# Performance work log

Hardware: AMD Instinct MI355X
Metric: run time of the kernel (lower is better)

The kernel has to match this reference:

```python
import jax, jax.numpy as jnp
import numpy as np
import itertools, math

B = 2048
DIM = 384
RES = 7
KEY_DIM = 16
HEADS = 8
RATIO = 4
NH_KD = KEY_DIM * HEADS          # 128
D = RATIO * KEY_DIM              # 64
DH = D * HEADS                   # 512
OUT_DIM = DIM                    # 384
RES2 = math.ceil(RES / 2)        # 4
N = RES * RES                    # 49
N2 = RES2 * RES2                 # 16
EPS = 1e-5
SCALE = KEY_DIM ** -0.5


def conv2d(x, w, b, stride=1, pad=0, groups=1):
    out = jax.lax.conv_general_dilated(
        x, w, (stride, stride), [(pad, pad), (pad, pad)],
        dimension_numbers=("NCHW", "OIHW", "NCHW"), feature_group_count=groups)
    return out + b[None, :, None, None]


def bn(x, p):
    # p: [4, C] = (gamma, beta, running_mean, running_var); inference-mode BN
    g, be, m, v = p[0], p[1], p[2], p[3]
    inv = jax.lax.rsqrt(v + EPS)
    return (x - m[None, :, None, None]) * (g * inv)[None, :, None, None] + be[None, :, None, None]


def avgpool2(x):
    # AvgPool2d(kernel=2, stride=2, padding=0)
    s = jax.lax.reduce_window(x, 0.0, jax.lax.add, (1, 1, 2, 2), (1, 1, 2, 2), "VALID")
    return s * 0.25


def _bias_idxs():
    points = list(itertools.product(range(RES), range(RES)))
    points_ = list(itertools.product(range(RES2), range(RES2)))
    stride = RES / RES2
    offsets, idxs = {}, []
    for p1 in points_:
        for p2 in points:
            off = (math.floor(abs(p1[0] * stride - p2[0])),
                   math.floor(abs(p1[1] * stride - p2[1])))
            if off not in offsets:
                offsets[off] = len(offsets)
            idxs.append(offsets[off])
    return np.array(idxs, dtype=np.int32).reshape(N2, N), len(offsets)


def _bn_params(k, c):
    k1, k2, k3, k4 = jax.random.split(k, 4)
    gamma = 1.0 + 0.1 * jax.random.normal(k1, (c,), jnp.float32)
    beta = 0.1 * jax.random.normal(k2, (c,), jnp.float32)
    mean = 0.1 * jax.random.normal(k3, (c,), jnp.float32)
    var = jax.random.uniform(k4, (c,), jnp.float32, 0.5, 1.5)
    return jnp.stack([gamma, beta, mean, var])


def _conv_w(k, shape):
    fan_in = shape[1] * shape[2] * shape[3]
    return jax.random.normal(k, shape, jnp.float32) / np.sqrt(fan_in)


def setup_inputs() -> dict:
    key = jax.random.key(0)
    ks = jax.random.split(key, 20)
    idxs_np, n_off = _bias_idxs()
    inp = {
        "x": jax.random.normal(ks[0], (B, DIM, RES, RES), jnp.float32),
        # LGQuery: depthwise 3x3 s2 + proj 1x1 + BN
        "qlw": _conv_w(ks[1], (DIM, 1, 3, 3)),
        "qlb": 0.01 * jax.random.normal(ks[2], (DIM,), jnp.float32),
        "qpw": _conv_w(ks[3], (NH_KD, DIM, 1, 1)),
        "qpb": 0.01 * jax.random.normal(ks[4], (NH_KD,), jnp.float32),
        "qbn": _bn_params(ks[5], NH_KD),
        # K branch: 1x1 conv + BN
        "kw": _conv_w(ks[6], (NH_KD, DIM, 1, 1)),
        "kb": 0.01 * jax.random.normal(ks[7], (NH_KD,), jnp.float32),
        "kbn": _bn_params(ks[8], NH_KD),
        # V branch: 1x1 conv + BN
        "vw": _conv_w(ks[9], (DH, DIM, 1, 1)),
        "vb": 0.01 * jax.random.normal(ks[10], (DH,), jnp.float32),
        "vbn": _bn_params(ks[11], DH),
        # v_local: depthwise 3x3 s2 + BN
        "vlw": _conv_w(ks[12], (DH, 1, 3, 3)),
        "vlb": 0.01 * jax.random.normal(ks[13], (DH,), jnp.float32),
        "vlbn": _bn_params(ks[14], DH),
        # proj: ReLU -> 1x1 conv -> BN
        "pw": _conv_w(ks[15], (OUT_DIM, DH, 1, 1)),
        "pb": 0.01 * jax.random.normal(ks[16], (OUT_DIM,), jnp.float32),
        "pbn": _bn_params(ks[17], OUT_DIM),
        # relative position biases + gather indices
        "ab": 0.02 * jax.random.normal(ks[18], (HEADS, n_off), jnp.float32),
        "bias_idxs": jnp.asarray(idxs_np),
    }
    return inp


def reference(x, qlw, qlb, qpw, qpb, qbn, kw, kb, kbn, vw, vb, vbn,
              vlw, vlb, vlbn, pw, pb, pbn, ab, bias_idxs):
    Bx = x.shape[0]
    # --- LGQuery ---
    local_q = conv2d(x, qlw, qlb, stride=2, pad=1, groups=DIM)   # [B,384,4,4]
    pool_q = avgpool2(x)                                         # [B,384,3,3]
    ph = local_q.shape[-2] - pool_q.shape[-2]
    pw_ = local_q.shape[-1] - pool_q.shape[-1]
    if ph > 0 or pw_ > 0:
        pool_q = jnp.pad(pool_q, ((0, 0), (0, 0), (0, ph), (0, pw_)))
    q_out = bn(conv2d(local_q + pool_q, qpw, qpb), qbn)          # [B,128,4,4]
    Hq, Wq = q_out.shape[-2], q_out.shape[-1]
    Nq = Hq * Wq
    # --- K / V ---
    k_out = bn(conv2d(x, kw, kb), kbn)                           # [B,128,7,7]
    Nk = k_out.shape[-2] * k_out.shape[-1]
    v_out = bn(conv2d(x, vw, vb), vbn)                           # [B,512,7,7]
    v_loc = bn(conv2d(v_out, vlw, vlb, stride=2, pad=1, groups=DH), vlbn)  # [B,512,4,4]
    # --- attention over tiny 16x49 matrices per head ---
    q = q_out.reshape(Bx, HEADS, KEY_DIM, Nq)                    # [B,H,kd,Nq]
    k = k_out.reshape(Bx, HEADS, KEY_DIM, Nk)                    # [B,H,kd,Nk]
    v = v_out.reshape(Bx, HEADS, D, Nk)                          # [B,H,d,Nk]
    attn = jnp.einsum("bhdq,bhdk->bhqk", q, k) * SCALE           # [B,H,16,49]
    if Nq == N2 and Nk == N:
        attn = attn + ab[:, bias_idxs]                           # gather -> [H,16,49]
    attn = jax.nn.softmax(attn, axis=-1)
    xa = jnp.einsum("bhqk,bhdk->bhdq", attn, v)                  # [B,H,d,Nq]
    out = xa.reshape(Bx, DH, Hq, Wq)                             # [B,512,4,4]
    ph2 = out.shape[-2] - v_loc.shape[-2]
    pw2 = out.shape[-1] - v_loc.shape[-1]
    if ph2 > 0 or pw2 > 0:
        v_loc = jnp.pad(v_loc, ((0, 0), (0, 0), (0, ph2), (0, pw2)))
    out = out + v_loc
    out = bn(conv2d(jax.nn.relu(out), pw, pb), pbn)              # [B,384,4,4]
    return out
```

## Files before the change

### kernel.cpp

```cpp
#include <hip/hip_runtime.h>
#include <hip/hip_bf16.h>


#define DIMC 384
#define NPOS 49
#define NHKD 128
#define DHC  512
#define OUTC 384

#define OFF_KW  0
#define OFF_VW  49152
#define OFF_QPW 245760
#define OFF_PW  294912
#define W_TOT   491520

#define XS_OFF 0
#define R0_OFF 19208
#define R1_OFF 27528
#define R2_OFF 32648
#define SMEM_ELEMS 40840

typedef __attribute__((ext_vector_type(8))) __bf16 bf16x8;
typedef __attribute__((ext_vector_type(4))) float f32x4;

static __device__ __forceinline__ __hip_bfloat16 f2b(float x) { return __float2bfloat16(x); }
static __device__ __forceinline__ float b2f(__hip_bfloat16 x) { return __bfloat162float(x); }
static __device__ __forceinline__ bf16x8 ld8(const __hip_bfloat16* p) { return *(const bf16x8*)p; }
static __device__ __forceinline__ f32x4 fzero() {
  f32x4 z; z[0] = 0.f; z[1] = 0.f; z[2] = 0.f; z[3] = 0.f; return z;
}
static __device__ __forceinline__ bf16x8 bzero() {
  bf16x8 z;
  #pragma unroll
  for (int j = 0; j < 8; ++j) z[j] = (__bf16)0.0f;
  return z;
}

static __device__ __forceinline__ void bn_so(const float* bn, int C, int ch,
                                             float convb, float& s, float& o) {
  float g  = bn[ch];
  float be = bn[C + ch];
  float mu = bn[2*C + ch];
  float va = bn[3*C + ch];
  s = g * rsqrtf(va + 1e-5f);
  o = be + (convb - mu) * s;
}

__global__ void prep_weights(const float* __restrict__ kw, const float* __restrict__ vw,
                             const float* __restrict__ qpw, const float* __restrict__ pw,
                             __hip_bfloat16* __restrict__ wsb) {
  for (int i = blockIdx.x * blockDim.x + threadIdx.x; i < W_TOT; i += gridDim.x * blockDim.x) {
    float v;
    if (i < OFF_VW)       v = kw[i - OFF_KW];
    else if (i < OFF_QPW) v = vw[i - OFF_VW];
    else if (i < OFF_PW)  v = qpw[i - OFF_QPW];
    else                  v = pw[i - OFF_PW];
    wsb[i] = f2b(v);
  }
}

__global__ __launch_bounds__(512, 4) void attn4d_kernel(
    const float* __restrict__ x,
    const float* __restrict__ qlw, const float* __restrict__ qlb,
    const float* __restrict__ qpb, const float* __restrict__ qbn,
    const float* __restrict__ kb,  const float* __restrict__ kbn,
    const float* __restrict__ vb,  const float* __restrict__ vbn,
    const float* __restrict__ vlw, const float* __restrict__ vlb,
    const float* __restrict__ vlbn,
    const float* __restrict__ pb,  const float* __restrict__ pbn,
    const float* __restrict__ ab,  const int* __restrict__ bidx,
    const __hip_bfloat16* __restrict__ wsb,
    int n_off, float* __restrict__ out)
{
  __shared__ __align__(16) __hip_bfloat16 smem[SMEM_ELEMS];
  __hip_bfloat16* xs    = smem + XS_OFF;
  __hip_bfloat16* vsm   = smem + XS_OFF;
  __hip_bfloat16* kt    = smem + R0_OFF;
  __hip_bfloat16* rout  = smem + R0_OFF;
  __hip_bfloat16* qsm   = smem + R1_OFF;
  __hip_bfloat16* qin   = smem + R2_OFF;
  __hip_bfloat16* attnS = smem + R2_OFF;

  const __hip_bfloat16* kwb  = wsb + OFF_KW;
  const __hip_bfloat16* vwb  = wsb + OFF_VW;
  const __hip_bfloat16* qpwb = wsb + OFF_QPW;
  const __hip_bfloat16* pwb  = wsb + OFF_PW;

  const int tid  = threadIdx.x;
  const int lane = tid & 63;
  const int wave = tid >> 6;
  const int quad = lane >> 4;
  const int l15  = lane & 15;
  const int b    = blockIdx.x;

  {
    const float* xg = x + (size_t)b * (DIMC * NPOS);
    for (int j = tid; j < NPOS * (DIMC / 8); j += 512) {
      const int n  = j % 49;
      const int c0 = (j / 49) * 8;
      union { bf16x8 v; __hip_bfloat16 h[8]; } u;
      #pragma unroll
      for (int k = 0; k < 8; ++k)
        u.h[k] = f2b(xg[(c0 + k) * 49 + n]);
      *(bf16x8*)&xs[n * 392 + c0] = u.v;
    }
  }
  __syncthreads();

  if (tid < DIMC) {
    const int c = tid;
    float xv[49];
    #pragma unroll
    for (int n = 0; n < 49; ++n) xv[n] = b2f(xs[n * 392 + c]);
    float wq[9];
    #pragma unroll
    for (int j = 0; j < 9; ++j) wq[j] = qlw[c * 9 + j];
    const float cb = qlb[c];
    #pragma unroll
    for (int oh = 0; oh < 4; ++oh) {
      #pragma unroll
      for (int ow = 0; ow < 4; ++ow) {
        float a = cb;
        #pragma unroll
        for (int kh = 0; kh < 3; ++kh) {
          const int ih = 2 * oh - 1 + kh;
          if (ih < 0 || ih > 6) continue;
          #pragma unroll
          for (int kwi = 0; kwi < 3; ++kwi) {
            const int iw = 2 * ow - 1 + kwi;
            if (iw < 0 || iw > 6) continue;
            a += wq[kh * 3 + kwi] * xv[ih * 7 + iw];
          }
        }
        if (oh < 3 && ow < 3)
          a += 0.25f * (xv[(2*oh)*7 + 2*ow] + xv[(2*oh)*7 + 2*ow + 1] +
                        xv[(2*oh+1)*7 + 2*ow] + xv[(2*oh+1)*7 + 2*ow + 1]);
        qin[(oh * 4 + ow) * 392 + c] = f2b(a);
      }
    }
  }
  __syncthreads();


  {
    const int mt = wave;
    f32x4 acc[4];
    #pragma unroll
    for (int nt = 0; nt < 4; ++nt) acc[nt] = fzero();
    for (int ks = 0; ks < 12; ++ks) {
      const int c0 = ks * 32 + quad * 8;
      bf16x8 a = ld8(&kwb[(mt * 16 + l15) * DIMC + c0]);
      bf16x8 z[4];
      #pragma unroll
      for (int nt = 0; nt < 3; ++nt) z[nt] = ld8(&xs[(nt * 16 + l15) * 392 + c0]);
      z[3] = (l15 == 0) ? ld8(&xs[48 * 392 + c0]) : bzero();
      #pragma unroll
      for (int nt = 0; nt < 4; ++nt)
        acc[nt] = __builtin_amdgcn_mfma_f32_16x16x32_bf16(a, z[nt], acc[nt], 0, 0, 0);
    }
    #pragma unroll
    for (int r = 0; r < 4; ++r) {
      const int oc = mt * 16 + quad * 4 + r;
      float s, o;
      bn_so(kbn, NHKD, oc, kb[oc], s, o);
      #pragma unroll
      for (int nt = 0; nt < 4; ++nt) {
        const int n = nt * 16 + l15;
        if (n < 49) kt[n * 136 + oc] = f2b(acc[nt][r] * s + o);
      }
    }
  }

  {
    const int mt = wave;
    f32x4 acc = fzero();
    for (int ks = 0; ks < 12; ++ks) {
      const int c0 = ks * 32 + quad * 8;
      bf16x8 bv = ld8(&qin[l15 * 392 + c0]);
      bf16x8 av = ld8(&qpwb[(mt * 16 + l15) * DIMC + c0]);
      acc = __builtin_amdgcn_mfma_f32_16x16x32_bf16(av, bv, acc, 0, 0, 0);
    }
    #pragma unroll
    for (int r = 0; r < 4; ++r) {
      const int oc = mt * 16 + quad * 4 + r;
      float s, o;
      bn_so(qbn, NHKD, oc, qpb[oc], s, o);
      const int kd = oc & 15;
      qsm[wave * 640 + l15 * 40 + kd] = f2b(acc[r] * s + o);
      qsm[wave * 640 + l15 * 40 + kd + 16] = f2b(0.f);
    }
  }

  f32x4 va[2][2][4];
  #pragma unroll
  for (int p = 0; p < 2; ++p)
    #pragma unroll
    for (int mt = 0; mt < 2; ++mt)
      #pragma unroll
      for (int nt = 0; nt < 4; ++nt) va[p][mt][nt] = fzero();
  {
    const int chb = wave * 32;
    for (int ks = 0; ks < 12; ++ks) {
      const int c0 = ks * 32 + quad * 8;
      bf16x8 z[4];
      #pragma unroll
      for (int nt = 0; nt < 3; ++nt) z[nt] = ld8(&xs[(nt * 16 + l15) * 392 + c0]);
      z[3] = (l15 == 0) ? ld8(&xs[48 * 392 + c0]) : bzero();
      #pragma unroll
      for (int p = 0; p < 2; ++p) {
        #pragma unroll
        for (int mt = 0; mt < 2; ++mt) {
          bf16x8 a = ld8(&vwb[(p * 256 + chb + mt * 16 + l15) * DIMC + c0]);
          #pragma unroll
          for (int nt = 0; nt < 4; ++nt)
            va[p][mt][nt] = __builtin_amdgcn_mfma_f32_16x16x32_bf16(a, z[nt], va[p][mt][nt], 0, 0, 0);
        }
      }
    }
  }
  __syncthreads();

  {
    __hip_bfloat16* vbw_ = vsm + wave * 2304;
    #pragma unroll
    for (int mt = 0; mt < 2; ++mt)
      #pragma unroll
      for (int r = 0; r < 4; ++r) {
        const int chl = mt * 16 + quad * 4 + r;
        const int gch = wave * 32 + chl;
        float s, o;
        bn_so(vbn, DHC, gch, vb[gch], s, o);
        #pragma unroll
        for (int nt = 0; nt < 4; ++nt)
          vbw_[chl * 72 + nt * 16 + l15] = f2b(va[0][mt][nt][r] * s + o);
      }
  }

  {
    const int h = wave;
    bf16x8 av = ld8(&qsm[h * 640 + l15 * 40 + quad * 8]);
    float p[4][4];
    #pragma unroll
    for (int t = 0; t < 4; ++t) {
      bf16x8 bv = bzero();
      if (quad < 2) bv = ld8(&kt[(t * 16 + l15) * 136 + h * 16 + quad * 8]);
      f32x4 lg = __builtin_amdgcn_mfma_f32_16x16x32_bf16(av, bv, fzero(), 0, 0, 0);
      #pragma unroll
      for (int r = 0; r < 4; ++r) {
        const int nq = quad * 4 + r;
        const int nk = t * 16 + l15;
        float val = -30000.f;
        if (nk < 49) val = lg[r] * 0.25f + ab[h * n_off + bidx[nq * 49 + nk]];
        p[t][r] = val;
      }
    }
    #pragma unroll
    for (int r = 0; r < 4; ++r) {
      float m = fmaxf(fmaxf(p[0][r], p[1][r]), fmaxf(p[2][r], p[3][r]));
      m = fmaxf(m, __shfl_xor(m, 1));
      m = fmaxf(m, __shfl_xor(m, 2));
      m = fmaxf(m, __shfl_xor(m, 4));
      m = fmaxf(m, __shfl_xor(m, 8));
      float e[4], sum = 0.f;
      #pragma unroll
      for (int t = 0; t < 4; ++t) { e[t] = __expf(p[t][r] - m); sum += e[t]; }
      sum += __shfl_xor(sum, 1);
      sum += __shfl_xor(sum, 2);
      sum += __shfl_xor(sum, 4);
      sum += __shfl_xor(sum, 8);
      const float inv = 1.f / sum;
      #pragma unroll
      for (int t = 0; t < 4; ++t) p[t][r] = e[t] * inv;
    }
    #pragma unroll
    for (int r = 0; r < 4; ++r) {
      const int nq = quad * 4 + r;
      #pragma unroll
      for (int t = 0; t < 4; ++t) {
        const int nk = t * 16 + l15;
        attnS[h * 1024 + nq * 64 + (nk ^ ((nq & 7) << 3))] = f2b(p[t][r]);
      }
    }
  }
  __syncthreads();

  #pragma unroll
  for (int p = 0; p < 2; ++p) {
    if (p == 1) {
      __hip_bfloat16* vbw_ = vsm + wave * 2304;
      #pragma unroll
      for (int mt = 0; mt < 2; ++mt)
        #pragma unroll
        for (int r = 0; r < 4; ++r) {
          const int chl = mt * 16 + quad * 4 + r;
          const int gch = 256 + wave * 32 + chl;
          float s, o;
          bn_so(vbn, DHC, gch, vb[gch], s, o);
          #pragma unroll
          for (int nt = 0; nt < 4; ++nt)
            vbw_[chl * 72 + nt * 16 + l15] = f2b(va[1][mt][nt][r] * s + o);
        }
    }

    {
      const int cl   = lane & 31;
      const int half = lane >> 5;
      const int gch  = p * 256 + wave * 32 + cl;
      const __hip_bfloat16* vrow = vsm + wave * 2304 + cl * 72;
      float wv[9];
      #pragma unroll
      for (int j = 0; j < 9; ++j) wv[j] = vlw[gch * 9 + j];
      float s, o;
      bn_so(vlbn, DHC, gch, vlb[gch], s, o);
      #pragma unroll
      for (int pp = 0; pp < 8; ++pp) {
        const int pos = half * 8 + pp;
        const int oh = pos >> 2, ow = pos & 3;
        float a = 0.f;
        #pragma unroll
        for (int kh = 0; kh < 3; ++kh) {
          const int ih = 2 * oh - 1 + kh;
          if (ih < 0 || ih > 6) continue;
          #pragma unroll
          for (int kwi = 0; kwi < 3; ++kwi) {
            const int iw = 2 * ow - 1 + kwi;
            if (iw < 0 || iw > 6) continue;
            a += wv[kh * 3 + kwi] * b2f(vrow[ih * 7 + iw]);
          }
        }
        rout[pos * 520 + gch] = f2b(a * s + o);
      }
    }

    {
      const int h = p * 4 + (wave >> 1);
      const __hip_bfloat16* vbw_ = vsm + wave * 2304;
      #pragma unroll
      for (int mt = 0; mt < 2; ++mt) {
        f32x4 acc = fzero();
        #pragma unroll
        for (int ks = 0; ks < 2; ++ks) {
          const int k0 = ks * 32 + quad * 8;
          bf16x8 av = ld8(&vbw_[(mt * 16 + l15) * 72 + k0]);
          bf16x8 bv = ld8(&attnS[h * 1024 + l15 * 64 + (k0 ^ ((l15 & 7) << 3))]);
          acc = __builtin_amdgcn_mfma_f32_16x16x32_bf16(av, bv, acc, 0, 0, 0);
        }
        #pragma unroll
        for (int r = 0; r < 4; ++r) {
          const int gch = p * 256 + wave * 32 + mt * 16 + quad * 4 + r;
          const int ad = l15 * 520 + gch;
          const float val = acc[r] + b2f(rout[ad]);
          rout[ad] = f2b(fmaxf(val, 0.f));
        }
      }
    }
  }
  __syncthreads();

  {
    const int mt0 = wave * 3;
    f32x4 acc[3];
    #pragma unroll
    for (int t = 0; t < 3; ++t) acc[t] = fzero();
    for (int ks = 0; ks < 16; ++ks) {
      const int c0 = ks * 32 + quad * 8;
      bf16x8 bv = ld8(&rout[l15 * 520 + c0]);
      #pragma unroll
      for (int t = 0; t < 3; ++t) {
        bf16x8 av = ld8(&pwb[((mt0 + t) * 16 + l15) * DHC + c0]);
        acc[t] = __builtin_amdgcn_mfma_f32_16x16x32_bf16(av, bv, acc[t], 0, 0, 0);
      }
    }
    float* outb = out + (size_t)b * (OUTC * 16);
    #pragma unroll
    for (int t = 0; t < 3; ++t) {
      #pragma unroll
      for (int r = 0; r < 4; ++r) {
        const int oc = (mt0 + t) * 16 + quad * 4 + r;
        float s, o;
        bn_so(pbn, OUTC, oc, pb[oc], s, o);
        outb[oc * 16 + l15] = acc[t][r] * s + o;
      }
    }
  }
}

extern "C" void kernel_launch(void* const* d_in, const int* in_sizes, int n_in,
                              void* d_out, int out_size, void* d_ws, size_t ws_size,
                              hipStream_t stream) {
  const float* x    = (const float*)d_in[0];
  const float* qlw  = (const float*)d_in[1];
  const float* qlb  = (const float*)d_in[2];
  const float* qpw  = (const float*)d_in[3];
  const float* qpb  = (const float*)d_in[4];
  const float* qbn  = (const float*)d_in[5];
  const float* kw   = (const float*)d_in[6];
  const float* kb   = (const float*)d_in[7];
  const float* kbn  = (const float*)d_in[8];
  const float* vw   = (const float*)d_in[9];
  const float* vb   = (const float*)d_in[10];
  const float* vbn  = (const float*)d_in[11];
  const float* vlw  = (const float*)d_in[12];
  const float* vlb  = (const float*)d_in[13];
  const float* vlbn = (const float*)d_in[14];
  const float* pw   = (const float*)d_in[15];
  const float* pb   = (const float*)d_in[16];
  const float* pbn  = (const float*)d_in[17];
  const float* ab   = (const float*)d_in[18];
  const int*   bidx = (const int*)d_in[19];
  const int n_off = in_sizes[18] / 8;
  const int Bn = in_sizes[0] / (DIMC * NPOS);

  __hip_bfloat16* wsb = (__hip_bfloat16*)d_ws;

  prep_weights<<<480, 256, 0, stream>>>(kw, vw, qpw, pw, wsb);
  attn4d_kernel<<<Bn, 512, 0, stream>>>(x, qlw, qlb, qpb, qbn, kb, kbn,
                                        vb, vbn, vlw, vlb, vlbn, pb, pbn,
                                        ab, bidx, wsb, n_off, (float*)d_out);
}
```

Measured before the change: 580.2 us.

## Precompute BN scale/offset and gathered attention bias in prep kernel; shrink LDS

Folds every batch-norm scale/shift and conv bias into a float2 table, and gathers the attention bias into a dense per-head table, both computed once in the weight-prep kernel rather than in every block. The main kernel reads these precomputed values, removing per-block rsqrt work and indirect gathers. It also shrinks the padded q buffer to lower LDS use, restructures the q depthwise conv to keep only three rows in registers, and preloads v rows as vector loads for the v-local conv. The cost is a slightly larger prep kernel and a different LDS layout.

```diff
diff --git a/kernel.cpp b/kernel.cpp
--- a/kernel.cpp
+++ b/kernel.cpp
@@ -13,12 +13,19 @@
 #define OFF_QPW 245760
 #define OFF_PW  294912
 #define W_TOT   491520
-
-#define XS_OFF 0
-#define R0_OFF 19208
-#define R1_OFF 27528
-#define R2_OFF 32648
-#define SMEM_ELEMS 40840
+#define BN_K  0
+#define BN_Q  128
+#define BN_V  256
+#define BN_VL 768
+#define BN_P  1280
+#define BN_TOT 1664
+#define ABF_ELEMS (8 * 784)
+
+#define XS_OFF   0
+#define KT_OFF   19208
+#define QSM_OFF  27912
+#define QIN_OFF  29960
+#define SMEM_ELEMS 38152
 
 typedef __attribute__((ext_vector_type(8))) __bf16 bf16x8;
 typedef __attribute__((ext_vector_type(4))) float f32x4;
@@ -36,20 +43,19 @@
   return z;
 }
 
-static __device__ __forceinline__ void bn_so(const float* bn, int C, int ch,
-                                             float convb, float& s, float& o) {
-  float g  = bn[ch];
-  float be = bn[C + ch];
-  float mu = bn[2*C + ch];
-  float va = bn[3*C + ch];
-  s = g * rsqrtf(va + 1e-5f);
-  o = be + (convb - mu) * s;
-}
-
 __global__ void prep_weights(const float* __restrict__ kw, const float* __restrict__ vw,
                              const float* __restrict__ qpw, const float* __restrict__ pw,
+                             const float* __restrict__ kb,  const float* __restrict__ kbn,
+                             const float* __restrict__ qpb, const float* __restrict__ qbn,
+                             const float* __restrict__ vb,  const float* __restrict__ vbn,
+                             const float* __restrict__ vlb, const float* __restrict__ vlbn,
+                             const float* __restrict__ pb,  const float* __restrict__ pbn,
+                             const float* __restrict__ ab,  const int* __restrict__ bidx,
+                             int n_off,
                              __hip_bfloat16* __restrict__ wsb) {
-  for (int i = blockIdx.x * blockDim.x + threadIdx.x; i < W_TOT; i += gridDim.x * blockDim.x) {
+  const int gid = blockIdx.x * blockDim.x + threadIdx.x;
+  const int stride = gridDim.x * blockDim.x;
+  for (int i = gid; i < W_TOT; i += stride) {
     float v;
     if (i < OFF_VW)       v = kw[i - OFF_KW];
     else if (i < OFF_QPW) v = vw[i - OFF_VW];
@@ -57,34 +63,47 @@
     else                  v = pw[i - OFF_PW];
     wsb[i] = f2b(v);
   }
+  float2* bnt = (float2*)(wsb + W_TOT);
+  for (int i = gid; i < BN_TOT; i += stride) {
+    const float *bn, *cb; int ch, C;
+    if (i < BN_Q)        { bn = kbn;  cb = kb;  ch = i;         C = NHKD; }
+    else if (i < BN_V)   { bn = qbn;  cb = qpb; ch = i - BN_Q;  C = NHKD; }
+    else if (i < BN_VL)  { bn = vbn;  cb = vb;  ch = i - BN_V;  C = DHC;  }
+    else if (i < BN_P)   { bn = vlbn; cb = vlb; ch = i - BN_VL; C = DHC;  }
+    else                 { bn = pbn;  cb = pb;  ch = i - BN_P;  C = OUTC; }
+    const float g = bn[ch], be = bn[C + ch], mu = bn[2*C + ch], va = bn[3*C + ch];
+    const float s = g * rsqrtf(va + 1e-5f);
+    bnt[i] = make_float2(s, be + (cb[ch] - mu) * s);
+  }
+  float* abf = (float*)((char*)bnt + BN_TOT * 8);
+  for (int i = gid; i < ABF_ELEMS; i += stride) {
+    const int h = i / 784, j = i - h * 784;
+    abf[i] = ab[h * n_off + bidx[j]];
+  }
 }
 
 __global__ __launch_bounds__(512, 4) void attn4d_kernel(
     const float* __restrict__ x,
     const float* __restrict__ qlw, const float* __restrict__ qlb,
-    const float* __restrict__ qpb, const float* __restrict__ qbn,
-    const float* __restrict__ kb,  const float* __restrict__ kbn,
-    const float* __restrict__ vb,  const float* __restrict__ vbn,
-    const float* __restrict__ vlw, const float* __restrict__ vlb,
-    const float* __restrict__ vlbn,
-    const float* __restrict__ pb,  const float* __restrict__ pbn,
-    const float* __restrict__ ab,  const int* __restrict__ bidx,
+    const float* __restrict__ vlw,
     const __hip_bfloat16* __restrict__ wsb,
-    int n_off, float* __restrict__ out)
+    float* __restrict__ out)
 {
   __shared__ __align__(16) __hip_bfloat16 smem[SMEM_ELEMS];
   __hip_bfloat16* xs    = smem + XS_OFF;
   __hip_bfloat16* vsm   = smem + XS_OFF;
-  __hip_bfloat16* kt    = smem + R0_OFF;
-  __hip_bfloat16* rout  = smem + R0_OFF;
-  __hip_bfloat16* qsm   = smem + R1_OFF;
-  __hip_bfloat16* qin   = smem + R2_OFF;
-  __hip_bfloat16* attnS = smem + R2_OFF;
+  __hip_bfloat16* kt    = smem + KT_OFF;
+  __hip_bfloat16* rout  = smem + KT_OFF;
+  __hip_bfloat16* qsm   = smem + QSM_OFF;
+  __hip_bfloat16* qin   = smem + QIN_OFF;
+  __hip_bfloat16* attnS = smem + QIN_OFF;
 
   const __hip_bfloat16* kwb  = wsb + OFF_KW;
   const __hip_bfloat16* vwb  = wsb + OFF_VW;
   const __hip_bfloat16* qpwb = wsb + OFF_QPW;
   const __hip_bfloat16* pwb  = wsb + OFF_PW;
+  const float2* bnt = (const float2*)(wsb + W_TOT);
+  const float*  abf = (const float*)((const char*)bnt + BN_TOT * 8);
 
   const int tid  = threadIdx.x;
   const int lane = tid & 63;
@@ -98,29 +117,219 @@
     for (int j = tid; j < NPOS * (DIMC / 8); j += 512) {
       const int n  = j % 49;
       const int c0 = (j / 49) * 8;
-      union { bf16x8 v; __hip_bfloat16 h[8]; } u;
+      bf16x8 v;
       #pragma unroll
       for (int k = 0; k < 8; ++k)
-        u.h[k] = f2b(xg[(c0 + k) * 49 + n]);
-      *(bf16x8*)&xs[n * 392 + c0] = u.v;
+        v[k] = (__bf16)(xg[(c0 + k) * 49 + n]);
+      *(bf16x8*)&xs[n * 392 + c0] = v;
     }
   }
   __syncthreads();
 
-  if (tid < DIMC) {
+  if (tid < 384) {
     const int c = tid;
-    float xv[49];
-    #pragma unroll
-    for (int n = 0; n < 49; ++n) xv[n] = b2f(xs[n * 392 + c]);
     float wq[9];
     #pragma unroll
     for (int j = 0; j < 9; ++j) wq[j] = qlw[c * 9 + j];
     const float cb = qlb[c];
     #pragma unroll
     for (int oh = 0; oh < 4; ++oh) {
+      float w[3][7];
+      #pragma unroll
+      for (int i = 0; i < 7; ++i) {
+        w[0][i] = (oh > 0) ? b2f(xs[((2*oh - 1) * 7 + i) * 392 + c]) : 0.f;
+        w[1][i] = b2f(xs[((2*oh) * 7 + i) * 392 + c]);
+        w[2][i] = (oh < 3) ? b2f(xs[((2*oh + 1) * 7 + i) * 392 + c]) : 0.f;
+      }
       #pragma unroll
       for (int ow = 0; ow < 4; ++ow) {
         float a = cb;
+        #pragma unroll
+        for (int kh = 0; kh < 3; ++kh) {
+          #pragma unroll
+          for (int kwi = 0; kwi < 3; ++kwi) {
+            const int iw = 2 * ow - 1 + kwi;
+            if (iw < 0 || iw > 6) continue;
+            a += wq[kh * 3 + kwi] * w[kh][iw];
+          }
+        }
+        if (oh < 3 && ow < 3)
+          a += 0.25f * (w[1][2*ow] + w[1][2*ow + 1] + w[2][2*ow] + w[2][2*ow + 1]);
+        qin[(oh * 4 + ow) * 392 + c] = f2b(a);
+      }
+    }
+  }
+  __syncthreads();
+
+
+  {
+    const int mt = wave;
+    f32x4 acc[4];
+    #pragma unroll
+    for (int nt = 0; nt < 4; ++nt) acc[nt] = fzero();
+    for (int ks = 0; ks < 12; ++ks) {
+      const int c0 = ks * 32 + quad * 8;
+      bf16x8 a = ld8(&kwb[(mt * 16 + l15) * DIMC + c0]);
+      bf16x8 z[4];
+      #pragma unroll
+      for (int nt = 0; nt < 3; ++nt) z[nt] = ld8(&xs[(nt * 16 + l15) * 392 + c0]);
+      z[3] = (l15 == 0) ? ld8(&xs[48 * 392 + c0]) : bzero();
+      #pragma unroll
+      for (int nt = 0; nt < 4; ++nt)
+        acc[nt] = __builtin_amdgcn_mfma_f32_16x16x32_bf16(a, z[nt], acc[nt], 0, 0, 0);
+    }
+    #pragma unroll
+    for (int r = 0; r < 4; ++r) {
+      const int oc = mt * 16 + quad * 4 + r;
+      const float2 so = bnt[BN_K + oc];
+      #pragma unroll
+      for (int nt = 0; nt < 4; ++nt) {
+        const int n = nt * 16 + l15;
+        if (n < 49) kt[n * 136 + oc] = f2b(acc[nt][r] * so.x + so.y);
+      }
+    }
+  }
+
+  {
+    const int mt = wave;
+    f32x4 acc = fzero();
+    for (int ks = 0; ks < 12; ++ks) {
+      const int c0 = ks * 32 + quad * 8;
+      bf16x8 bv = ld8(&qin[l15 * 392 + c0]);
+      bf16x8 av = ld8(&qpwb[(mt * 16 + l15) * DIMC + c0]);
+      acc = __builtin_amdgcn_mfma_f32_16x16x32_bf16(av, bv, acc, 0, 0, 0);
+    }
+    #pragma unroll
+    for (int r = 0; r < 4; ++r) {
+      const int oc = mt * 16 + quad * 4 + r;
+      const float2 so = bnt[BN_Q + oc];
+      qsm[mt * 256 + l15 * 16 + (oc & 15)] = f2b(acc[r] * so.x + so.y);
+    }
+  }
+
+  f32x4 va[2][2][4];
+  #pragma unroll
+  for (int p = 0; p < 2; ++p)
+    #pragma unroll
+    for (int mt = 0; mt < 2; ++mt)
+      #pragma unroll
+      for (int nt = 0; nt < 4; ++nt) va[p][mt][nt] = fzero();
+  {
+    const int chb = wave * 32;
+    for (int ks = 0; ks < 12; ++ks) {
+      const int c0 = ks * 32 + quad * 8;
+      bf16x8 z[4];
+      #pragma unroll
+      for (int nt = 0; nt < 3; ++nt) z[nt] = ld8(&xs[(nt * 16 + l15) * 392 + c0]);
+      z[3] = (l15 == 0) ? ld8(&xs[48 * 392 + c0]) : bzero();
+      #pragma unroll
+      for (int p = 0; p < 2; ++p) {
+        #pragma unroll
+        for (int mt = 0; mt < 2; ++mt) {
+          bf16x8 a = ld8(&vwb[(p * 256 + chb + mt * 16 + l15) * DIMC + c0]);
+          #pragma unroll
+          for (int nt = 0; nt < 4; ++nt)
+            va[p][mt][nt] = __builtin_amdgcn_mfma_f32_16x16x32_bf16(a, z[nt], va[p][mt][nt], 0, 0, 0);
+        }
+      }
+    }
+  }
+  __syncthreads();
+
+  {
+    __hip_bfloat16* vbw_ = vsm + wave * 2304;
+    #pragma unroll
+    for (int mt = 0; mt < 2; ++mt)
+      #pragma unroll
+      for (int r = 0; r < 4; ++r) {
+        const int chl = mt * 16 + quad * 4 + r;
+        const float2 so = bnt[BN_V + wave * 32 + chl];
+        #pragma unroll
+        for (int nt = 0; nt < 4; ++nt)
+          vbw_[chl * 72 + nt * 16 + l15] = f2b(va[0][mt][nt][r] * so.x + so.y);
+      }
+  }
+
+  {
+    const int h = wave;
+    bf16x8 av = (quad < 2) ? ld8(&qsm[h * 256 + l15 * 16 + quad * 8]) : bzero();
+    float p[4][4];
+    #pragma unroll
+    for (int t = 0; t < 4; ++t) {
+      bf16x8 bv = (quad < 2) ? ld8(&kt[(t * 16 + l15) * 136 + h * 16 + quad * 8]) : bzero();
+      f32x4 lg = __builtin_amdgcn_mfma_f32_16x16x32_bf16(av, bv, fzero(), 0, 0, 0);
+      #pragma unroll
+      for (int r = 0; r < 4; ++r) {
+        const int nq = quad * 4 + r;
+        const int nk = t * 16 + l15;
+        float val = -30000.f;
+        if (nk < 49) val = lg[r] * 0.25f + abf[h * 784 + nq * 49 + nk];
+        p[t][r] = val;
+      }
+    }
+    #pragma unroll
+    for (int r = 0; r < 4; ++r) {
+      float m = fmaxf(fmaxf(p[0][r], p[1][r]), fmaxf(p[2][r], p[3][r]));
+      m = fmaxf(m, __shfl_xor(m, 1));
+      m = fmaxf(m, __shfl_xor(m, 2));
+      m = fmaxf(m, __shfl_xor(m, 4));
+      m = fmaxf(m, __shfl_xor(m, 8));
+      float e[4], sum = 0.f;
+      #pragma unroll
+      for (int t = 0; t < 4; ++t) { e[t] = __expf(p[t][r] - m); sum += e[t]; }
+      sum += __shfl_xor(sum, 1);
+      sum += __shfl_xor(sum, 2);
+      sum += __shfl_xor(sum, 4);
+      sum += __shfl_xor(sum, 8);
+      const float inv = 1.f / sum;
+      #pragma unroll
+      for (int t = 0; t < 4; ++t) p[t][r] = e[t] * inv;
+    }
+    #pragma unroll
+    for (int r = 0; r < 4; ++r) {
+      const int nq = quad * 4 + r;
+      #pragma unroll
+      for (int t = 0; t < 4; ++t) {
+        const int nk = t * 16 + l15;
+        attnS[h * 1024 + nq * 64 + (nk ^ ((nq & 7) << 3))] = f2b(p[t][r]);
+      }
+    }
+  }
+  __syncthreads();
+
+  #pragma unroll
+  for (int p = 0; p < 2; ++p) {
+    if (p == 1) {
+      __hip_bfloat16* vbw_ = vsm + wave * 2304;
+      #pragma unroll
+      for (int mt = 0; mt < 2; ++mt)
+        #pragma unroll
+        for (int r = 0; r < 4; ++r) {
+          const int chl = mt * 16 + quad * 4 + r;
+          const float2 so = bnt[BN_V + 256 + wave * 32 + chl];
+          #pragma unroll
+          for (int nt = 0; nt < 4; ++nt)
+            vbw_[chl * 72 + nt * 16 + l15] = f2b(va[1][mt][nt][r] * so.x + so.y);
+        }
+    }
+
+    {
+      const int cl   = lane & 31;
+      const int half = lane >> 5;
+      const int gch  = p * 256 + wave * 32 + cl;
+      const __hip_bfloat16* vrow = vsm + wave * 2304 + cl * 72;
+      bf16x8 rv[7];
+      #pragma unroll
+      for (int t = 0; t < 7; ++t) rv[t] = ld8(vrow + t * 8);
+      float wv[9];
+      #pragma unroll
+      for (int j = 0; j < 9; ++j) wv[j] = vlw[gch * 9 + j];
+      const float2 so = bnt[BN_VL + gch];
+      #pragma unroll
+      for (int pp = 0; pp < 8; ++pp) {
+        const int pos = half * 8 + pp;
+        const int oh = pos >> 2, ow = pos & 3;
+        float a = 0.f;
         #pragma unroll
         for (int kh = 0; kh < 3; ++kh) {
           const int ih = 2 * oh - 1 + kh;
@@ -129,206 +338,11 @@
           for (int kwi = 0; kwi < 3; ++kwi) {
             const int iw = 2 * ow - 1 + kwi;
             if (iw < 0 || iw > 6) continue;
-            a += wq[kh * 3 + kwi] * xv[ih * 7 + iw];
+            const int e = ih * 7 + iw;
+            a += wv[kh * 3 + kwi] * (float)rv[e >> 3][e & 7];
           }
         }
-        if (oh < 3 && ow < 3)
-          a += 0.25f * (xv[(2*oh)*7 + 2*ow] + xv[(2*oh)*7 + 2*ow + 1] +
-                        xv[(2*oh+1)*7 + 2*ow] + xv[(2*oh+1)*7 + 2*ow + 1]);
-        qin[(oh * 4 + ow) * 392 + c] = f2b(a);
-      }
-    }
-  }
-  __syncthreads();
-
-
-  {
-    const int mt = wave;
-    f32x4 acc[4];
-    #pragma unroll
-    for (int nt = 0; nt < 4; ++nt) acc[nt] = fzero();
-    for (int ks = 0; ks < 12; ++ks) {
-      const int c0 = ks * 32 + quad * 8;
-      bf16x8 a = ld8(&kwb[(mt * 16 + l15) * DIMC + c0]);
-      bf16x8 z[4];
-      #pragma unroll
-      for (int nt = 0; nt < 3; ++nt) z[nt] = ld8(&xs[(nt * 16 + l15) * 392 + c0]);
-      z[3] = (l15 == 0) ? ld8(&xs[48 * 392 + c0]) : bzero();
-      #pragma unroll
-      for (int nt = 0; nt < 4; ++nt)
-        acc[nt] = __builtin_amdgcn_mfma_f32_16x16x32_bf16(a, z[nt], acc[nt], 0, 0, 0);
-    }
-    #pragma unroll
-    for (int r = 0; r < 4; ++r) {
-      const int oc = mt * 16 + quad * 4 + r;
-      float s, o;
-      bn_so(kbn, NHKD, oc, kb[oc], s, o);
-      #pragma unroll
-      for (int nt = 0; nt < 4; ++nt) {
-        const int n = nt * 16 + l15;
-        if (n < 49) kt[n * 136 + oc] = f2b(acc[nt][r] * s + o);
-      }
-    }
-  }
-
-  {
-    const int mt = wave;
-    f32x4 acc = fzero();
-    for (int ks = 0; ks < 12; ++ks) {
-      const int c0 = ks * 32 + quad * 8;
-      bf16x8 bv = ld8(&qin[l15 * 392 + c0]);
-      bf16x8 av = ld8(&qpwb[(mt * 16 + l15) * DIMC + c0]);
-      acc = __builtin_amdgcn_mfma_f32_16x16x32_bf16(av, bv, acc, 0, 0, 0);
-    }
-    #pragma unroll
-    for (int r = 0; r < 4; ++r) {
-      const int oc = mt * 16 + quad * 4 + r;
-      float s, o;
-      bn_so(qbn, NHKD, oc, qpb[oc], s, o);
-      const int kd = oc & 15;
-      qsm[wave * 640 + l15 * 40 + kd] = f2b(acc[r] * s + o);
-      qsm[wave * 640 + l15 * 40 + kd + 16] = f2b(0.f);
-    }
-  }
-
-  f32x4 va[2][2][4];
-  #pragma unroll
-  for (int p = 0; p < 2; ++p)
-    #pragma unroll
-    for (int mt = 0; mt < 2; ++mt)
-      #pragma unroll
-      for (int nt = 0; nt < 4; ++nt) va[p][mt][nt] = fzero();
-  {
-    const int chb = wave * 32;
-    for (int ks = 0; ks < 12; ++ks) {
-      const int c0 = ks * 32 + quad * 8;
-      bf16x8 z[4];
-      #pragma unroll
-      for (int nt = 0; nt < 3; ++nt) z[nt] = ld8(&xs[(nt * 16 + l15) * 392 + c0]);
-      z[3] = (l15 == 0) ? ld8(&xs[48 * 392 + c0]) : bzero();
-      #pragma unroll
-      for (int p = 0; p < 2; ++p) {
-        #pragma unroll
-        for (int mt = 0; mt < 2; ++mt) {
-          bf16x8 a = ld8(&vwb[(p * 256 + chb + mt * 16 + l15) * DIMC + c0]);
-          #pragma unroll
-          for (int nt = 0; nt < 4; ++nt)
-            va[p][mt][nt] = __builtin_amdgcn_mfma_f32_16x16x32_bf16(a, z[nt], va[p][mt][nt], 0, 0, 0);
-        }
-      }
-    }
-  }
-  __syncthreads();
-
-  {
-    __hip_bfloat16* vbw_ = vsm + wave * 2304;
-    #pragma unroll
-    for (int mt = 0; mt < 2; ++mt)
-      #pragma unroll
-      for (int r = 0; r < 4; ++r) {
-        const int chl = mt * 16 + quad * 4 + r;
-        const int gch = wave * 32 + chl;
-        float s, o;
-        bn_so(vbn, DHC, gch, vb[gch], s, o);
-        #pragma unroll
-        for (int nt = 0; nt < 4; ++nt)
-          vbw_[chl * 72 + nt * 16 + l15] = f2b(va[0][mt][nt][r] * s + o);
-      }
-  }
-
-  {
-    const int h = wave;
-    bf16x8 av = ld8(&qsm[h * 640 + l15 * 40 + quad * 8]);
-    float p[4][4];
-    #pragma unroll
-    for (int t = 0; t < 4; ++t) {
-      bf16x8 bv = bzero();
-      if (quad < 2) bv = ld8(&kt[(t * 16 + l15) * 136 + h * 16 + quad * 8]);
-      f32x4 lg = __builtin_amdgcn_mfma_f32_16x16x32_bf16(av, bv, fzero(), 0, 0, 0);
-      #pragma unroll
-      for (int r = 0; r < 4; ++r) {
-        const int nq = quad * 4 + r;
-        const int nk = t * 16 + l15;
-        float val = -30000.f;
-        if (nk < 49) val = lg[r] * 0.25f + ab[h * n_off + bidx[nq * 49 + nk]];
-        p[t][r] = val;
-      }
-    }
-    #pragma unroll
-    for (int r = 0; r < 4; ++r) {
-      float m = fmaxf(fmaxf(p[0][r], p[1][r]), fmaxf(p[2][r], p[3][r]));
-      m = fmaxf(m, __shfl_xor(m, 1));
-      m = fmaxf(m, __shfl_xor(m, 2));
-      m = fmaxf(m, __shfl_xor(m, 4));
-      m = fmaxf(m, __shfl_xor(m, 8));
-      float e[4], sum = 0.f;
-      #pragma unroll
-      for (int t = 0; t < 4; ++t) { e[t] = __expf(p[t][r] - m); sum += e[t]; }
-      sum += __shfl_xor(sum, 1);
-      sum += __shfl_xor(sum, 2);
-      sum += __shfl_xor(sum, 4);
-      sum += __shfl_xor(sum, 8);
-      const float inv = 1.f / sum;
-      #pragma unroll
-      for (int t = 0; t < 4; ++t) p[t][r] = e[t] * inv;
-    }
-    #pragma unroll
-    for (int r = 0; r < 4; ++r) {
-      const int nq = quad * 4 + r;
-      #pragma unroll
-      for (int t = 0; t < 4; ++t) {
-        const int nk = t * 16 + l15;
-        attnS[h * 1024 + nq * 64 + (nk ^ ((nq & 7) << 3))] = f2b(p[t][r]);
-      }
-    }
-  }
-  __syncthreads();
-
-  #pragma unroll
-  for (int p = 0; p < 2; ++p) {
-    if (p == 1) {
-      __hip_bfloat16* vbw_ = vsm + wave * 2304;
-      #pragma unroll
-      for (int mt = 0; mt < 2; ++mt)
-        #pragma unroll
-        for (int r = 0; r < 4; ++r) {
-          const int chl = mt * 16 + quad * 4 + r;
-          const int gch = 256 + wave * 32 + chl;
-          float s, o;
-          bn_so(vbn, DHC, gch, vb[gch], s, o);
-          #pragma unroll
-          for (int nt = 0; nt < 4; ++nt)
-            vbw_[chl * 72 + nt * 16 + l15] = f2b(va[1][mt][nt][r] * s + o);
-        }
-    }
-
-    {
-      const int cl   = lane & 31;
-      const int half = lane >> 5;
-      const int gch  = p * 256 + wave * 32 + cl;
-      const __hip_bfloat16* vrow = vsm + wave * 2304 + cl * 72;
-      float wv[9];
-      #pragma unroll
-      for (int j = 0; j < 9; ++j) wv[j] = vlw[gch * 9 + j];
-      float s, o;
-      bn_so(vlbn, DHC, gch, vlb[gch], s, o);
-      #pragma unroll
-      for (int pp = 0; pp < 8; ++pp) {
-        const int pos = half * 8 + pp;
-        const int oh = pos >> 2, ow = pos & 3;
-        float a = 0.f;
-        #pragma unroll
-        for (int kh = 0; kh < 3; ++kh) {
-          const int ih = 2 * oh - 1 + kh;
-          if (ih < 0 || ih > 6) continue;
-          #pragma unroll
-          for (int kwi = 0; kwi < 3; ++kwi) {
-            const int iw = 2 * ow - 1 + kwi;
-            if (iw < 0 || iw > 6) continue;
-            a += wv[kh * 3 + kwi] * b2f(vrow[ih * 7 + iw]);
-          }
-        }
-        rout[pos * 520 + gch] = f2b(a * s + o);
+        rout[pos * 520 + gch] = f2b(a * so.x + so.y);
       }
     }
 
@@ -341,9 +355,9 @@
         #pragma unroll
         for (int ks = 0; ks < 2; ++ks) {
           const int k0 = ks * 32 + quad * 8;
-          bf16x8 av = ld8(&vbw_[(mt * 16 + l15) * 72 + k0]);
-          bf16x8 bv = ld8(&attnS[h * 1024 + l15 * 64 + (k0 ^ ((l15 & 7) << 3))]);
-          acc = __builtin_amdgcn_mfma_f32_16x16x32_bf16(av, bv, acc, 0, 0, 0);
+          bf16x8 avv = ld8(&vbw_[(mt * 16 + l15) * 72 + k0]);
+          bf16x8 bvv = ld8(&attnS[h * 1024 + l15 * 64 + (k0 ^ ((l15 & 7) << 3))]);
+          acc = __builtin_amdgcn_mfma_f32_16x16x32_bf16(avv, bvv, acc, 0, 0, 0);
         }
         #pragma unroll
         for (int r = 0; r < 4; ++r) {
@@ -373,15 +387,13 @@
     }
     float* outb = out + (size_t)b * (OUTC * 16);
     #pragma unroll
-    for (int t = 0; t < 3; ++t) {
+    for (int t = 0; t < 3; ++t)
       #pragma unroll
       for (int r = 0; r < 4; ++r) {
         const int oc = (mt0 + t) * 16 + quad * 4 + r;
-        float s, o;
-        bn_so(pbn, OUTC, oc, pb[oc], s, o);
-        outb[oc * 16 + l15] = acc[t][r] * s + o;
-      }
-    }
+        const float2 so = bnt[BN_P + oc];
+        outb[oc * 16 + l15] = acc[t][r] * so.x + so.y;
+      }
   }
 }
 
@@ -413,8 +425,8 @@
 
   __hip_bfloat16* wsb = (__hip_bfloat16*)d_ws;
 
-  prep_weights<<<480, 256, 0, stream>>>(kw, vw, qpw, pw, wsb);
-  attn4d_kernel<<<Bn, 512, 0, stream>>>(x, qlw, qlb, qpb, qbn, kb, kbn,
-                                        vb, vbn, vlw, vlb, vlbn, pb, pbn,
-                                        ab, bidx, wsb, n_off, (float*)d_out);
+  prep_weights<<<480, 256, 0, stream>>>(kw, vw, qpw, pw,
+                                        kb, kbn, qpb, qbn, vb, vbn,
+                                        vlb, vlbn, pb, pbn, ab, bidx, n_off, wsb);
+  attn4d_kernel<<<Bn, 512, 0, stream>>>(x, qlw, qlb, vlw, wsb, (float*)d_out);
 }
```

Result: no change. 591.3 us (+1.9%).
